# Kernel tuning notes

Measured on AMD Instinct MI355X. Metric: run time of the kernel, lower is better.

## Reference

```python
import jax, jax.numpy as jnp
import numpy as np

B, S, D, N = 128, 1024, 512, 784  # batch, state_dim, image_feature_dim, spatial positions


def setup_inputs() -> dict:
    key = jax.random.key(0)
    ks = jax.random.split(key, 6)
    s = lambda fan_in: 1.0 / np.sqrt(fan_in)
    return {
        "in_state": jax.random.normal(ks[0], (B, S), jnp.float32),
        "image": jax.random.normal(ks[1], (B, D, N), jnp.float32),
        "Wq": jax.random.normal(ks[2], (D, S), jnp.float32) * s(S),
        "bq": jnp.zeros((D,), jnp.float32),
        "Wc": jax.random.normal(ks[3], (D, 2 * D), jnp.float32) * s(2 * D),
        "bc": jnp.zeros((D,), jnp.float32),
        "Wa": jax.random.normal(ks[4], (1, D), jnp.float32) * s(D),
        "ba": jnp.zeros((1,), jnp.float32),
        "Wo": jax.random.normal(ks[5], (S, D), jnp.float32) * s(D),
        "bo": jnp.zeros((S,), jnp.float32),
    }


def reference(in_state, image, Wq, bq, Wc, bc, Wa, ba, Wo, bo):
    # query: [B, D]
    query = in_state @ Wq.T + bq
    # broadcast multiply over spatial positions: [B, D, N]
    qimg = query[:, :, None] * image
    # cat along channel dim then permute -> [B, N, 2D]
    feats = jnp.concatenate([qimg, image], axis=1).transpose(0, 2, 1)
    # concat linear: [B, N, D]
    c = feats @ Wc.T + bc
    # attention logits: [B, N]
    logits = (c @ Wa.T + ba)[..., 0]
    attn = jax.nn.softmax(logits, axis=1)  # softmax over spatial dim
    # weighted sum over spatial positions: [B, D]
    pooled = jnp.einsum("bn,bdn->bd", attn, image)
    return pooled @ Wo.T + bo
```

## Files before the change

kernel.cpp:

```cpp
#include <hip/hip_runtime.h>
#include <math.h>

#define BB 128
#define SS 1024
#define DD 512
#define NN 784
#define NCHK 4
#define NC 196

__device__ __forceinline__ float wave_reduce_sum(float x) {
#pragma unroll
  for (int m = 32; m > 0; m >>= 1) x += __shfl_xor(x, m, 64);
  return x;
}
__device__ __forceinline__ float wave_reduce_max(float x) {
#pragma unroll
  for (int m = 32; m > 0; m >>= 1) x = fmaxf(x, __shfl_xor(x, m, 64));
  return x;
}

__global__ void k1_v(const float* __restrict__ Wa, const float* __restrict__ Wc,
                     float* __restrict__ v) {
  int k = blockIdx.x * 256 + threadIdx.x;
  int j0 = blockIdx.y * 32;
  float acc = 0.f;
#pragma unroll
  for (int j = 0; j < 32; ++j)
    acc += Wa[j0 + j] * Wc[(size_t)(j0 + j) * (2 * DD) + k];
  atomicAdd(&v[k], acc);
}

__global__ void k2_w(const float* __restrict__ in_state, const float* __restrict__ Wq,
                     const float* __restrict__ bq, const float* __restrict__ v,
                     float* __restrict__ w) {
  __shared__ float st[SS];
  int b = blockIdx.y;
  int t = threadIdx.x, lane = t & 63, wv = t >> 6;
  ((float4*)st)[t] = ((const float4*)(in_state + (size_t)b * SS))[t];
  __syncthreads();
  const float4* st4 = (const float4*)st;
  float4 s0 = st4[lane], s1 = st4[lane + 64], s2 = st4[lane + 128], s3 = st4[lane + 192];
  int d0 = blockIdx.x * 32 + wv * 8;
  float acc[8];
#pragma unroll
  for (int r = 0; r < 8; ++r) {
    const float4* q4 = (const float4*)(Wq + (size_t)(d0 + r) * SS);
    float4 a0 = q4[lane], a1 = q4[lane + 64], a2 = q4[lane + 128], a3 = q4[lane + 192];
    acc[r] = a0.x * s0.x + a0.y * s0.y + a0.z * s0.z + a0.w * s0.w
           + a1.x * s1.x + a1.y * s1.y + a1.z * s1.z + a1.w * s1.w
           + a2.x * s2.x + a2.y * s2.y + a2.z * s2.z + a2.w * s2.w
           + a3.x * s3.x + a3.y * s3.y + a3.z * s3.z + a3.w * s3.w;
  }
#pragma unroll
  for (int r = 0; r < 8; ++r) acc[r] = wave_reduce_sum(acc[r]);
  if (lane == 0) {
#pragma unroll
    for (int r = 0; r < 8; ++r) {
      int d = d0 + r;
      w[(size_t)b * DD + d] = (acc[r] + bq[d]) * v[d] + v[DD + d];
    }
  }
}

__global__ void k3_fused(const float* __restrict__ image, const float* __restrict__ w,
                         float* __restrict__ P_part, float* __restrict__ mZ_part) {
  __shared__ float w_lds[DD];
  __shared__ float4 red[8][49];
  __shared__ float4 u_lds[49];
  __shared__ float p_s[DD];
  int b = blockIdx.y, c = blockIdx.x;
  int t = threadIdx.x, lane = t & 63, wv = t >> 6;
  w_lds[t] = w[(size_t)b * DD + t];
  __syncthreads();
  const float4* img4 = (const float4*)image + (size_t)b * DD * 196;
  int d0 = wv * 64;
  const float4* pbase = img4 + (size_t)d0 * 196 + c * 49 + (lane < 49 ? lane : 48);
  float4 acc = {0, 0, 0, 0};
#pragma unroll 8
  for (int i = 0; i < 64; ++i) {
    float4 x = pbase[i * 196];
    float wd = w_lds[d0 + i];
    acc.x += wd * x.x; acc.y += wd * x.y; acc.z += wd * x.z; acc.w += wd * x.w;
  }
  if (lane < 49) red[wv][lane] = acc;
  __syncthreads();
  if (wv == 0) {
    float4 l4 = {0, 0, 0, 0};
    float lm = -1e30f;
    if (lane < 49) {
#pragma unroll
      for (int v8 = 0; v8 < 8; ++v8) {
        float4 r = red[v8][lane];
        l4.x += r.x; l4.y += r.y; l4.z += r.z; l4.w += r.w;
      }
      lm = fmaxf(fmaxf(l4.x, l4.y), fmaxf(l4.z, l4.w));
    }
    float m = wave_reduce_max(lm);
    float zs = 0.f;
    if (lane < 49) {
      float4 u4;
      u4.x = __expf(l4.x - m); u4.y = __expf(l4.y - m);
      u4.z = __expf(l4.z - m); u4.w = __expf(l4.w - m);
      zs = u4.x + u4.y + u4.z + u4.w;
      u_lds[lane] = u4;
    }
    float Z = wave_reduce_sum(zs);
    if (lane == 0) {
      mZ_part[((size_t)b * NCHK + c) * 2 + 0] = m;
      mZ_part[((size_t)b * NCHK + c) * 2 + 1] = Z;
    }
  }
  __syncthreads();
  float4 u4 = {0, 0, 0, 0};
  if (lane < 49) u4 = u_lds[lane];
#pragma unroll 4
  for (int i = 0; i < 64; ++i) {
    float part = 0.f;
    if (lane < 49) {
      float4 x = pbase[i * 196];
      part = u4.x * x.x + u4.y * x.y + u4.z * x.z + u4.w * x.w;
    }
    part = wave_reduce_sum(part);
    if (lane == 0) p_s[d0 + i] = part;
  }
  P_part[((size_t)b * NCHK + c) * DD + d0 + lane] = p_s[d0 + lane];
}

__global__ void k5_combine(const float* __restrict__ P_part, const float* __restrict__ mZ_part,
                           float* __restrict__ pooled) {
  int b = blockIdx.x, t = threadIdx.x;
  float mc[NCHK], Zc[NCHK];
  float M = -1e30f;
#pragma unroll
  for (int c = 0; c < NCHK; ++c) {
    mc[c] = mZ_part[((size_t)b * NCHK + c) * 2 + 0];
    Zc[c] = mZ_part[((size_t)b * NCHK + c) * 2 + 1];
    M = fmaxf(M, mc[c]);
  }
  float Z = 0.f, al[NCHK];
#pragma unroll
  for (int c = 0; c < NCHK; ++c) { al[c] = __expf(mc[c] - M); Z += al[c] * Zc[c]; }
  float inv = 1.0f / Z;
  float4 s = {0, 0, 0, 0};
#pragma unroll
  for (int c = 0; c < NCHK; ++c) {
    float4 p = ((const float4*)P_part)[((size_t)b * NCHK + c) * 128 + t];
    s.x += al[c] * p.x; s.y += al[c] * p.y; s.z += al[c] * p.z; s.w += al[c] * p.w;
  }
  s.x *= inv; s.y *= inv; s.z *= inv; s.w *= inv;
  ((float4*)pooled)[(size_t)b * 128 + t] = s;
}

__global__ void k6_out(const float* __restrict__ pooled, const float* __restrict__ Wo,
                       const float* __restrict__ bo, float* __restrict__ out) {
  __shared__ float p_s[DD];
  int b = blockIdx.y, t = threadIdx.x, lane = t & 63, wv = t >> 6;
  ((float2*)p_s)[t] = ((const float2*)(pooled + (size_t)b * DD))[t];
  __syncthreads();
  const float4* p4 = (const float4*)p_s;
  float4 p0 = p4[lane], p1 = p4[lane + 64];
  int s0 = blockIdx.x * 32 + wv * 8;
  float acc[8];
#pragma unroll
  for (int r = 0; r < 8; ++r) {
    const float4* wo4 = (const float4*)(Wo + (size_t)(s0 + r) * DD);
    float4 x0 = wo4[lane], x1 = wo4[lane + 64];
    acc[r] = x0.x * p0.x + x0.y * p0.y + x0.z * p0.z + x0.w * p0.w
           + x1.x * p1.x + x1.y * p1.y + x1.z * p1.z + x1.w * p1.w;
  }
#pragma unroll
  for (int r = 0; r < 8; ++r) acc[r] = wave_reduce_sum(acc[r]);
  if (lane == 0) {
#pragma unroll
    for (int r = 0; r < 8; ++r) out[(size_t)b * SS + s0 + r] = acc[r] + bo[s0 + r];
  }
}

extern "C" void kernel_launch(void* const* d_in, const int* in_sizes, int n_in,
                              void* d_out, int out_size, void* d_ws, size_t ws_size,
                              hipStream_t stream) {
  const float* in_state = (const float*)d_in[0];
  const float* image    = (const float*)d_in[1];
  const float* Wq       = (const float*)d_in[2];
  const float* bq       = (const float*)d_in[3];
  const float* Wc       = (const float*)d_in[4];
  const float* Wa       = (const float*)d_in[6];
  const float* Wo       = (const float*)d_in[8];
  const float* bo       = (const float*)d_in[9];
  float* out = (float*)d_out;

  float* ws      = (float*)d_ws;
  float* v       = ws;
  float* w       = v + 2 * DD;
  float* P_part  = w + BB * DD;
  float* mZ_part = P_part + (size_t)BB * NCHK * DD;
  float* pooled  = mZ_part + (size_t)BB * NCHK * 2;

  hipMemsetAsync(v, 0, 2 * DD * sizeof(float), stream);
  k1_v<<<dim3(4, 16), 256, 0, stream>>>(Wa, Wc, v);
  k2_w<<<dim3(16, BB), 256, 0, stream>>>(in_state, Wq, bq, v, w);
  k3_fused<<<dim3(NCHK, BB), 512, 0, stream>>>(image, w, P_part, mZ_part);
  k5_combine<<<BB, 128, 0, stream>>>(P_part, mZ_part, pooled);
  k6_out<<<dim3(32, BB), 256, 0, stream>>>(pooled, Wo, bo, out);
}
```

Before: 371.8 us.

## Split fused attention kernel into logits, softmax, and pooling passes

Replaces the single fused logits/softmax/pool kernel, which read each image batch twice inside one block using a strided pattern with 49-of-64 active lanes, with three kernels. The logits pass splits the channel dimension into 8 chunks and streams the image contiguously, accumulating per-position partial logits through LDS atomics. A separate softmax kernel normalises the logits. A pooling kernel then reads the image again row-contiguously, with each wave reducing whole rows against the attention weights. The per-chunk softmax combine step goes away, but the image is still read twice from memory, two extra launches are added, and the LDS atomics may contend.

```diff
diff --git a/kernel.cpp b/kernel.cpp
--- a/kernel.cpp
+++ b/kernel.cpp
@@ -5,8 +5,9 @@
 #define SS 1024
 #define DD 512
 #define NN 784
-#define NCHK 4
-#define NC 196
+#define NQ 196
+#define QCH 8
+#define DC 64
 
 __device__ __forceinline__ float wave_reduce_sum(float x) {
 #pragma unroll
@@ -62,93 +63,98 @@
   }
 }
 
-__global__ void k3_fused(const float* __restrict__ image, const float* __restrict__ w,
-                         float* __restrict__ P_part, float* __restrict__ mZ_part) {
-  __shared__ float w_lds[DD];
-  __shared__ float4 red[8][49];
-  __shared__ float4 u_lds[49];
-  __shared__ float p_s[DD];
-  int b = blockIdx.y, c = blockIdx.x;
+__global__ void k3a_logits(const float* __restrict__ image, const float* __restrict__ w,
+                           float* __restrict__ Lpart) {
+  __shared__ float wl[DC];
+  __shared__ float l[4][NQ];
+  int b = blockIdx.y, q = blockIdx.x;
+  int t = threadIdx.x;
+  if (t < DC) wl[t] = w[(size_t)b * DD + q * DC + t];
+  float* lf = &l[0][0];
+  lf[t] = 0.f; lf[t + 256] = 0.f; lf[t + 512] = 0.f;
+  if (t < 16) lf[t + 768] = 0.f;
+  __syncthreads();
+  const float4* src = (const float4*)image + ((size_t)b * DD * NN + (size_t)q * DC * NN) / 4;
+  int s = t % NQ;
+  int d = t / NQ;
+#pragma unroll 7
+  for (int i = 0; i < 49; ++i) {
+    float4 x = src[t + 256 * i];
+    float wd = wl[d];
+    atomicAdd(&l[0][s], wd * x.x);
+    atomicAdd(&l[1][s], wd * x.y);
+    atomicAdd(&l[2][s], wd * x.z);
+    atomicAdd(&l[3][s], wd * x.w);
+    s += 60; d += 1;
+    int ov = (s >= NQ);
+    s -= NQ * ov; d += ov;
+  }
+  __syncthreads();
+  if (t < NQ) {
+    float4 o;
+    o.x = l[0][t]; o.y = l[1][t]; o.z = l[2][t]; o.w = l[3][t];
+    ((float4*)Lpart)[((size_t)b * QCH + q) * NQ + t] = o;
+  }
+}
+
+__global__ void k3b_softmax(const float* __restrict__ Lpart, float* __restrict__ attn) {
+  __shared__ float red[8];
+  int b = blockIdx.x, t = threadIdx.x, lane = t & 63, wv = t >> 6;
+  float4 l4 = {0.f, 0.f, 0.f, 0.f};
+  if (t < NQ) {
+#pragma unroll
+    for (int q = 0; q < QCH; ++q) {
+      float4 p = ((const float4*)Lpart)[((size_t)b * QCH + q) * NQ + t];
+      l4.x += p.x; l4.y += p.y; l4.z += p.z; l4.w += p.w;
+    }
+  }
+  float m = (t < NQ) ? fmaxf(fmaxf(l4.x, l4.y), fmaxf(l4.z, l4.w)) : -1e30f;
+  m = wave_reduce_max(m);
+  if (lane == 0) red[wv] = m;
+  __syncthreads();
+  float M = fmaxf(fmaxf(red[0], red[1]), fmaxf(red[2], red[3]));
+  float4 u = {0.f, 0.f, 0.f, 0.f};
+  float zs = 0.f;
+  if (t < NQ) {
+    u.x = __expf(l4.x - M); u.y = __expf(l4.y - M);
+    u.z = __expf(l4.z - M); u.w = __expf(l4.w - M);
+    zs = u.x + u.y + u.z + u.w;
+  }
+  zs = wave_reduce_sum(zs);
+  if (lane == 0) red[4 + wv] = zs;
+  __syncthreads();
+  float Z = red[4] + red[5] + red[6] + red[7];
+  float inv = 1.0f / Z;
+  if (t < NQ) {
+    u.x *= inv; u.y *= inv; u.z *= inv; u.w *= inv;
+    ((float4*)attn)[(size_t)b * NQ + t] = u;
+  }
+}
+
+__global__ void k3c_pool(const float* __restrict__ image, const float* __restrict__ attn,
+                         float* __restrict__ pooled) {
+  int b = blockIdx.y, g = blockIdx.x;
   int t = threadIdx.x, lane = t & 63, wv = t >> 6;
-  w_lds[t] = w[(size_t)b * DD + t];
-  __syncthreads();
-  const float4* img4 = (const float4*)image + (size_t)b * DD * 196;
-  int d0 = wv * 64;
-  const float4* pbase = img4 + (size_t)d0 * 196 + c * 49 + (lane < 49 ? lane : 48);
-  float4 acc = {0, 0, 0, 0};
-#pragma unroll 8
-  for (int i = 0; i < 64; ++i) {
-    float4 x = pbase[i * 196];
-    float wd = w_lds[d0 + i];
-    acc.x += wd * x.x; acc.y += wd * x.y; acc.z += wd * x.z; acc.w += wd * x.w;
-  }
-  if (lane < 49) red[wv][lane] = acc;
-  __syncthreads();
-  if (wv == 0) {
-    float4 l4 = {0, 0, 0, 0};
-    float lm = -1e30f;
-    if (lane < 49) {
-#pragma unroll
-      for (int v8 = 0; v8 < 8; ++v8) {
-        float4 r = red[v8][lane];
-        l4.x += r.x; l4.y += r.y; l4.z += r.z; l4.w += r.w;
-      }
-      lm = fmaxf(fmaxf(l4.x, l4.y), fmaxf(l4.z, l4.w));
+  const float4* a4 = (const float4*)attn + (size_t)b * NQ;
+  float4 A0 = a4[lane], A1 = a4[lane + 64], A2 = a4[lane + 128];
+  float4 A3 = {0.f, 0.f, 0.f, 0.f};
+  if (lane < 4) A3 = a4[lane + 192];
+  int d0 = g * 64 + wv * 8;
+  const float4* src = (const float4*)image + (size_t)b * DD * NQ;
+#pragma unroll 4
+  for (int r = 0; r < 8; ++r) {
+    const float4* row = src + (size_t)(d0 + r) * NQ;
+    float4 x0 = row[lane], x1 = row[lane + 64], x2 = row[lane + 128];
+    float acc = A0.x * x0.x + A0.y * x0.y + A0.z * x0.z + A0.w * x0.w
+              + A1.x * x1.x + A1.y * x1.y + A1.z * x1.z + A1.w * x1.w
+              + A2.x * x2.x + A2.y * x2.y + A2.z * x2.z + A2.w * x2.w;
+    if (lane < 4) {
+      float4 x3 = row[lane + 192];
+      acc += A3.x * x3.x + A3.y * x3.y + A3.z * x3.z + A3.w * x3.w;
     }
-    float m = wave_reduce_max(lm);
-    float zs = 0.f;
-    if (lane < 49) {
-      float4 u4;
-      u4.x = __expf(l4.x - m); u4.y = __expf(l4.y - m);
-      u4.z = __expf(l4.z - m); u4.w = __expf(l4.w - m);
-      zs = u4.x + u4.y + u4.z + u4.w;
-      u_lds[lane] = u4;
-    }
-    float Z = wave_reduce_sum(zs);
-    if (lane == 0) {
-      mZ_part[((size_t)b * NCHK + c) * 2 + 0] = m;
-      mZ_part[((size_t)b * NCHK + c) * 2 + 1] = Z;
-    }
-  }
-  __syncthreads();
-  float4 u4 = {0, 0, 0, 0};
-  if (lane < 49) u4 = u_lds[lane];
-#pragma unroll 4
-  for (int i = 0; i < 64; ++i) {
-    float part = 0.f;
-    if (lane < 49) {
-      float4 x = pbase[i * 196];
-      part = u4.x * x.x + u4.y * x.y + u4.z * x.z + u4.w * x.w;
-    }
-    part = wave_reduce_sum(part);
-    if (lane == 0) p_s[d0 + i] = part;
-  }
-  P_part[((size_t)b * NCHK + c) * DD + d0 + lane] = p_s[d0 + lane];
-}
-
-__global__ void k5_combine(const float* __restrict__ P_part, const float* __restrict__ mZ_part,
-                           float* __restrict__ pooled) {
-  int b = blockIdx.x, t = threadIdx.x;
-  float mc[NCHK], Zc[NCHK];
-  float M = -1e30f;
-#pragma unroll
-  for (int c = 0; c < NCHK; ++c) {
-    mc[c] = mZ_part[((size_t)b * NCHK + c) * 2 + 0];
-    Zc[c] = mZ_part[((size_t)b * NCHK + c) * 2 + 1];
-    M = fmaxf(M, mc[c]);
-  }
-  float Z = 0.f, al[NCHK];
-#pragma unroll
-  for (int c = 0; c < NCHK; ++c) { al[c] = __expf(mc[c] - M); Z += al[c] * Zc[c]; }
-  float inv = 1.0f / Z;
-  float4 s = {0, 0, 0, 0};
-#pragma unroll
-  for (int c = 0; c < NCHK; ++c) {
-    float4 p = ((const float4*)P_part)[((size_t)b * NCHK + c) * 128 + t];
-    s.x += al[c] * p.x; s.y += al[c] * p.y; s.z += al[c] * p.z; s.w += al[c] * p.w;
-  }
-  s.x *= inv; s.y *= inv; s.z *= inv; s.w *= inv;
-  ((float4*)pooled)[(size_t)b * 128 + t] = s;
+    acc = wave_reduce_sum(acc);
+    if (lane == 0) pooled[(size_t)b * DD + d0 + r] = acc;
+  }
 }
 
 __global__ void k6_out(const float* __restrict__ pooled, const float* __restrict__ Wo,
@@ -189,17 +195,18 @@
   const float* bo       = (const float*)d_in[9];
   float* out = (float*)d_out;
 
-  float* ws      = (float*)d_ws;
-  float* v       = ws;
-  float* w       = v + 2 * DD;
-  float* P_part  = w + BB * DD;
-  float* mZ_part = P_part + (size_t)BB * NCHK * DD;
-  float* pooled  = mZ_part + (size_t)BB * NCHK * 2;
+  float* ws     = (float*)d_ws;
+  float* v      = ws;
+  float* w      = v + 2 * DD;
+  float* Lpart  = w + (size_t)BB * DD;
+  float* attn   = Lpart + (size_t)BB * QCH * NN;
+  float* pooled = attn + (size_t)BB * NN;
 
   hipMemsetAsync(v, 0, 2 * DD * sizeof(float), stream);
   k1_v<<<dim3(4, 16), 256, 0, stream>>>(Wa, Wc, v);
   k2_w<<<dim3(16, BB), 256, 0, stream>>>(in_state, Wq, bq, v, w);
-  k3_fused<<<dim3(NCHK, BB), 512, 0, stream>>>(image, w, P_part, mZ_part);
-  k5_combine<<<BB, 128, 0, stream>>>(P_part, mZ_part, pooled);
+  k3a_logits<<<dim3(QCH, BB), 256, 0, stream>>>(image, w, Lpart);
+  k3b_softmax<<<BB, 256, 0, stream>>>(Lpart, attn);
+  k3c_pool<<<dim3(8, BB), 512, 0, stream>>>(image, attn, pooled);
   k6_out<<<dim3(32, BB), 256, 0, stream>>>(pooled, Wo, bo, out);
 }
```

Result: slower. 548.1 us (+47.4%).

## Stage image chunk in LDS and split spatial dim into 14 chunks

Applied to the files above, without the earlier changes.

The fused attention kernel now splits the spatial dimension into 14 chunks of 56 positions instead of 4. Each block loads its full 512x56 image tile into LDS once, computes the logits with wave reductions, and reuses the LDS copy for the softmax-weighted pooling, so the image is no longer read twice from global memory. This gives more blocks (14x128), which should raise occupancy. In exchange it uses about 120KB of LDS per block, spends many shuffle reductions per column, writes more partial results, and makes the combine step sum over 14 chunks.

```diff
diff --git a/kernel.cpp b/kernel.cpp
--- a/kernel.cpp
+++ b/kernel.cpp
@@ -5,8 +5,9 @@
 #define SS 1024
 #define DD 512
 #define NN 784
-#define NCHK 4
-#define NC 196
+#define NQ 196
+#define CH 14
+#define CSL 14
 
 __device__ __forceinline__ float wave_reduce_sum(float x) {
 #pragma unroll
@@ -62,89 +63,88 @@
   }
 }
 
-__global__ void k3_fused(const float* __restrict__ image, const float* __restrict__ w,
-                         float* __restrict__ P_part, float* __restrict__ mZ_part) {
-  __shared__ float w_lds[DD];
-  __shared__ float4 red[8][49];
-  __shared__ float4 u_lds[49];
-  __shared__ float p_s[DD];
+__global__ __launch_bounds__(512, 2) void k3_chunk(
+    const float* __restrict__ image, const float* __restrict__ w,
+    float* __restrict__ P_part, float* __restrict__ mZ_part) {
+  __shared__ float4 xs[DD][CSL + 1];
+  __shared__ float4 lred[8][CSL];
   int b = blockIdx.y, c = blockIdx.x;
   int t = threadIdx.x, lane = t & 63, wv = t >> 6;
-  w_lds[t] = w[(size_t)b * DD + t];
-  __syncthreads();
-  const float4* img4 = (const float4*)image + (size_t)b * DD * 196;
-  int d0 = wv * 64;
-  const float4* pbase = img4 + (size_t)d0 * 196 + c * 49 + (lane < 49 ? lane : 48);
-  float4 acc = {0, 0, 0, 0};
-#pragma unroll 8
-  for (int i = 0; i < 64; ++i) {
-    float4 x = pbase[i * 196];
-    float wd = w_lds[d0 + i];
-    acc.x += wd * x.x; acc.y += wd * x.y; acc.z += wd * x.z; acc.w += wd * x.w;
-  }
-  if (lane < 49) red[wv][lane] = acc;
-  __syncthreads();
-  if (wv == 0) {
-    float4 l4 = {0, 0, 0, 0};
-    float lm = -1e30f;
-    if (lane < 49) {
-#pragma unroll
-      for (int v8 = 0; v8 < 8; ++v8) {
-        float4 r = red[v8][lane];
-        l4.x += r.x; l4.y += r.y; l4.z += r.z; l4.w += r.w;
-      }
-      lm = fmaxf(fmaxf(l4.x, l4.y), fmaxf(l4.z, l4.w));
+  const char* base = (const char*)image + (size_t)b * DD * (NN * 4) + c * (CSL * 16);
+#pragma unroll
+  for (int k = 0; k < CSL; ++k) {
+    int f = t + k * 512;
+    int r = f / CSL, j = f % CSL;
+    float4 x = *(const float4*)(base + (size_t)r * (NN * 4) + j * 16);
+    xs[r][j] = x;
+  }
+  float wt = w[(size_t)b * DD + t];
+  __syncthreads();
+#pragma unroll
+  for (int j = 0; j < CSL; ++j) {
+    float4 x = xs[t][j];
+    float4 s;
+    s.x = wave_reduce_sum(wt * x.x);
+    s.y = wave_reduce_sum(wt * x.y);
+    s.z = wave_reduce_sum(wt * x.z);
+    s.w = wave_reduce_sum(wt * x.w);
+    if (lane == 0) lred[wv][j] = s;
+  }
+  __syncthreads();
+  float4 l[CSL];
+#pragma unroll
+  for (int j = 0; j < CSL; ++j) {
+    float4 s = lred[0][j];
+#pragma unroll
+    for (int v8 = 1; v8 < 8; ++v8) {
+      float4 p = lred[v8][j];
+      s.x += p.x; s.y += p.y; s.z += p.z; s.w += p.w;
     }
-    float m = wave_reduce_max(lm);
-    float zs = 0.f;
-    if (lane < 49) {
-      float4 u4;
-      u4.x = __expf(l4.x - m); u4.y = __expf(l4.y - m);
-      u4.z = __expf(l4.z - m); u4.w = __expf(l4.w - m);
-      zs = u4.x + u4.y + u4.z + u4.w;
-      u_lds[lane] = u4;
-    }
-    float Z = wave_reduce_sum(zs);
-    if (lane == 0) {
-      mZ_part[((size_t)b * NCHK + c) * 2 + 0] = m;
-      mZ_part[((size_t)b * NCHK + c) * 2 + 1] = Z;
-    }
-  }
-  __syncthreads();
-  float4 u4 = {0, 0, 0, 0};
-  if (lane < 49) u4 = u_lds[lane];
-#pragma unroll 4
-  for (int i = 0; i < 64; ++i) {
-    float part = 0.f;
-    if (lane < 49) {
-      float4 x = pbase[i * 196];
-      part = u4.x * x.x + u4.y * x.y + u4.z * x.z + u4.w * x.w;
-    }
-    part = wave_reduce_sum(part);
-    if (lane == 0) p_s[d0 + i] = part;
-  }
-  P_part[((size_t)b * NCHK + c) * DD + d0 + lane] = p_s[d0 + lane];
+    l[j] = s;
+  }
+  float m = -1e30f;
+#pragma unroll
+  for (int j = 0; j < CSL; ++j)
+    m = fmaxf(m, fmaxf(fmaxf(l[j].x, l[j].y), fmaxf(l[j].z, l[j].w)));
+  float Z = 0.f;
+#pragma unroll
+  for (int j = 0; j < CSL; ++j) {
+    l[j].x = __expf(l[j].x - m); l[j].y = __expf(l[j].y - m);
+    l[j].z = __expf(l[j].z - m); l[j].w = __expf(l[j].w - m);
+    Z += l[j].x + l[j].y + l[j].z + l[j].w;
+  }
+  float acc = 0.f;
+#pragma unroll
+  for (int j = 0; j < CSL; ++j) {
+    float4 x = xs[t][j];
+    acc += l[j].x * x.x + l[j].y * x.y + l[j].z * x.z + l[j].w * x.w;
+  }
+  P_part[((size_t)b * CH + c) * DD + t] = acc;
+  if (t == 0) {
+    mZ_part[((size_t)b * CH + c) * 2 + 0] = m;
+    mZ_part[((size_t)b * CH + c) * 2 + 1] = Z;
+  }
 }
 
 __global__ void k5_combine(const float* __restrict__ P_part, const float* __restrict__ mZ_part,
                            float* __restrict__ pooled) {
   int b = blockIdx.x, t = threadIdx.x;
-  float mc[NCHK], Zc[NCHK];
+  float mc[CH], Zc[CH];
   float M = -1e30f;
 #pragma unroll
-  for (int c = 0; c < NCHK; ++c) {
-    mc[c] = mZ_part[((size_t)b * NCHK + c) * 2 + 0];
-    Zc[c] = mZ_part[((size_t)b * NCHK + c) * 2 + 1];
+  for (int c = 0; c < CH; ++c) {
+    mc[c] = mZ_part[((size_t)b * CH + c) * 2 + 0];
+    Zc[c] = mZ_part[((size_t)b * CH + c) * 2 + 1];
     M = fmaxf(M, mc[c]);
   }
-  float Z = 0.f, al[NCHK];
-#pragma unroll
-  for (int c = 0; c < NCHK; ++c) { al[c] = __expf(mc[c] - M); Z += al[c] * Zc[c]; }
+  float Z = 0.f, al[CH];
+#pragma unroll
+  for (int c = 0; c < CH; ++c) { al[c] = __expf(mc[c] - M); Z += al[c] * Zc[c]; }
   float inv = 1.0f / Z;
   float4 s = {0, 0, 0, 0};
 #pragma unroll
-  for (int c = 0; c < NCHK; ++c) {
-    float4 p = ((const float4*)P_part)[((size_t)b * NCHK + c) * 128 + t];
+  for (int c = 0; c < CH; ++c) {
+    float4 p = ((const float4*)P_part)[((size_t)b * CH + c) * 128 + t];
     s.x += al[c] * p.x; s.y += al[c] * p.y; s.z += al[c] * p.z; s.w += al[c] * p.w;
   }
   s.x *= inv; s.y *= inv; s.z *= inv; s.w *= inv;
@@ -192,14 +192,14 @@
   float* ws      = (float*)d_ws;
   float* v       = ws;
   float* w       = v + 2 * DD;
-  float* P_part  = w + BB * DD;
-  float* mZ_part = P_part + (size_t)BB * NCHK * DD;
-  float* pooled  = mZ_part + (size_t)BB * NCHK * 2;
+  float* P_part  = w + (size_t)BB * DD;
+  float* mZ_part = P_part + (size_t)BB * CH * DD;
+  float* pooled  = mZ_part + (size_t)BB * CH * 2;
 
   hipMemsetAsync(v, 0, 2 * DD * sizeof(float), stream);
   k1_v<<<dim3(4, 16), 256, 0, stream>>>(Wa, Wc, v);
   k2_w<<<dim3(16, BB), 256, 0, stream>>>(in_state, Wq, bq, v, w);
-  k3_fused<<<dim3(NCHK, BB), 512, 0, stream>>>(image, w, P_part, mZ_part);
+  k3_chunk<<<dim3(CH, BB), 512, 0, stream>>>(image, w, P_part, mZ_part);
   k5_combine<<<BB, 128, 0, stream>>>(P_part, mZ_part, pooled);
   k6_out<<<dim3(32, BB), 256, 0, stream>>>(pooled, Wo, bo, out);
 }
```

Measured after the change: 403.9 us. +8.6%, slower.
